# Kernel tuning notes

Hardware: AMD Instinct MI355X
Metric: run time of the kernel (lower is better)

## Reference

```python
import jax, jax.numpy as jnp
import numpy as np

SL, BS, D, H = 2048, 4, 512, 8
NH = D // H  # per-head dim (nhid)
SCALE = np.float32(1.0 / np.sqrt(NH))


def setup_inputs() -> dict:
    key = jax.random.key(0)
    ks = jax.random.split(key, 8)
    s = np.float32(0.02)
    return {
        "input_tensor": jax.random.normal(ks[0], (SL, BS, D), jnp.float32),
        "keys_vector": jax.random.normal(ks[1], (SL, BS, D), jnp.float32),
        "values_vector": jax.random.normal(ks[2], (SL, BS, D), jnp.float32),
        # learned projections: query/keys/values -> num_heads*nhid, plus output proj
        "Wq": jax.random.normal(ks[3], (D, D), jnp.float32) * s,
        "bq": jnp.zeros((D,), jnp.float32),
        "Wk": jax.random.normal(ks[4], (D, D), jnp.float32) * s,
        "bk": jnp.zeros((D,), jnp.float32),
        "Wv": jax.random.normal(ks[5], (D, D), jnp.float32) * s,
        "bv": jnp.zeros((D,), jnp.float32),
        "Wo": jax.random.normal(ks[6], (D, D), jnp.float32) * s,
        "bo": jnp.zeros((D,), jnp.float32),
    }


def reference(input_tensor, keys_vector, values_vector, Wq, bq, Wk, bk, Wv, bv, Wo, bo):
    # Vectorized equivalent of the per-step Python loop with incremental mask
    # (mask=True): query step i attends to keys 0..i -> causal attention.
    q = (input_tensor @ Wq + bq).reshape(SL, BS, H, NH)   # [q,b,h,n]
    k = (keys_vector @ Wk + bk).reshape(SL, BS, H, NH)    # [s,b,h,n]
    v = (values_vector @ Wv + bv).reshape(SL, BS, H, NH)  # [s,b,h,n]
    scores = jnp.einsum('qbhn,sbhn->qsbh', q, k) * SCALE  # [q,s,b,h]
    causal = jnp.tril(jnp.ones((SL, SL), dtype=bool))     # allow s <= q
    scores = jnp.where(causal[:, :, None, None], scores, jnp.float32(-1e9))
    w = jax.nn.softmax(scores, axis=1)                    # softmax over keys s
    out = jnp.einsum('qsbh,sbhn->qbhn', w, v).reshape(SL, BS, D)
    return out @ Wo + bo                                  # [q,b,D]
```

## Files before the change

kernel.cpp:

```cpp
#include <hip/hip_runtime.h>

typedef __attribute__((ext_vector_type(8))) short short8;
typedef __attribute__((ext_vector_type(4))) short short4v;
typedef __attribute__((ext_vector_type(4))) float f32x4;
typedef __attribute__((ext_vector_type(2))) unsigned int uint2v;

constexpr int SL = 2048, BS = 4, D = 512, H = 8, NH = 64;
constexpr int M_ROWS = SL * BS;
constexpr float SCALE = 0.125f;
constexpr float LOG2E = 1.44269504088896340736f;

__device__ __forceinline__ unsigned short f2bf(float f) {
  union { float f; unsigned u; } v; v.f = f;
  unsigned r = v.u + 0x7FFFu + ((v.u >> 16) & 1u);
  return (unsigned short)(r >> 16);
}

__device__ __forceinline__ unsigned cvt_pk_bf16(float a, float b) {
  unsigned r;
  asm("v_cvt_pk_bf16_f32 %0, %1, %2" : "=v"(r) : "v"(a), "v"(b));
  return r;
}

__device__ __forceinline__ float fast_exp2(float x) {
  float r;
  asm("v_exp_f32 %0, %1" : "=v"(r) : "v"(x));
  return r;
}

__device__ __forceinline__ void gl16(const void* g, void* l) {
  __builtin_amdgcn_global_load_lds(
      (const __attribute__((address_space(1))) unsigned int*)g,
      (__attribute__((address_space(3))) unsigned int*)l, 16, 0, 0);
}

__global__ __launch_bounds__(256) void prep_wt(
    const float* __restrict__ w0, const float* __restrict__ w1,
    const float* __restrict__ w2, const float* __restrict__ w3,
    unsigned short* __restrict__ wtb) {
  __shared__ float tl[64][65];
  const int tid = threadIdx.x;
  const int wi = blockIdx.x >> 6, t6 = blockIdx.x & 63;
  const int k0 = (t6 >> 3) * 64, n0 = (t6 & 7) * 64;
  const float* W = wi == 0 ? w0 : (wi == 1 ? w1 : (wi == 2 ? w2 : w3));
  unsigned short* WT = wtb + (size_t)wi * D * D;

#pragma unroll
  for (int i = 0; i < 4; ++i) {
    int k = (tid >> 4) + i * 16, n4 = (tid & 15) * 4;
    f32x4 v = *reinterpret_cast<const f32x4*>(&W[(size_t)(k0 + k) * D + n0 + n4]);
#pragma unroll
    for (int j = 0; j < 4; ++j) tl[n4 + j][k] = v[j];
  }
  __syncthreads();
#pragma unroll
  for (int i = 0; i < 2; ++i) {
    int n = (tid >> 3) + i * 32, k8 = (tid & 7) * 8;
    union { unsigned u[4]; short8 s; } pk;
#pragma unroll
    for (int j = 0; j < 4; ++j)
      pk.u[j] = cvt_pk_bf16(tl[n][k8 + 2 * j], tl[n][k8 + 2 * j + 1]);
    *reinterpret_cast<short8*>(&WT[(size_t)(n0 + n) * D + k0 + k8]) = pk.s;
  }
}

template <bool A_BF16, int OUT_MODE>
__device__ __forceinline__ void gemm_bt_body(const void* __restrict__ Ap,
                                             const unsigned short* __restrict__ BT,
                                             const float* __restrict__ bias,
                                             void* __restrict__ Outp, float scale,
                                             unsigned short* smem) {
  const int tid = threadIdx.x;
  const int brow = blockIdx.x * 128;
  const int bcol = blockIdx.y * 128;
  const int lane = tid & 63;
  const int wid = tid >> 6;
  const int wr = (wid >> 1) * 64;
  const int wc = (wid & 1) * 64;
  const int r = lane & 15;
  const int g = lane >> 4;

  auto a_buf = [&](int b) { return smem + b * 16384; };
  auto b_buf = [&](int b) { return smem + b * 16384 + 8192; };

  f32x4 acc[4][4];
#pragma unroll
  for (int m = 0; m < 4; ++m)
#pragma unroll
    for (int n = 0; n < 4; ++n) acc[m][n] = f32x4{0.f, 0.f, 0.f, 0.f};

  auto STAGE_B = [&](int kt, int bsel) {
    unsigned short* bl = b_buf(bsel);
#pragma unroll
    for (int j = 0; j < 4; ++j) {
      int c = j * 256 + tid;
      int row = c >> 3, c8 = (c & 7) ^ (row & 7);
      gl16(&BT[(size_t)(bcol + row) * D + kt + c8 * 8], &bl[c * 8]);
    }
  };
  auto STAGE_A_LDS = [&](int kt, int bsel) {
    const unsigned short* A = (const unsigned short*)Ap;
    unsigned short* al = a_buf(bsel);
#pragma unroll
    for (int j = 0; j < 4; ++j) {
      int c = j * 256 + tid;
      int row = c >> 3, c8 = (c & 7) ^ (row & 7);
      gl16(&A[(size_t)(brow + row) * D + kt + c8 * 8], &al[c * 8]);
    }
  };
  auto A_LOAD = [&](int kt, f32x4 (&va)[4][2]) {
    const float* A = (const float*)Ap;
#pragma unroll
    for (int j = 0; j < 4; ++j) {
      int c = j * 256 + tid;
      int row = c >> 3, c8 = (c & 7) ^ (row & 7);
      const float* ap = &A[(size_t)(brow + row) * D + kt + c8 * 8];
      va[j][0] = *reinterpret_cast<const f32x4*>(ap);
      va[j][1] = *reinterpret_cast<const f32x4*>(ap + 4);
    }
  };
  auto A_WRITE = [&](f32x4 (&va)[4][2], int bsel) {
    unsigned short* al = a_buf(bsel);
#pragma unroll
    for (int j = 0; j < 4; ++j) {
      int c = j * 256 + tid;
      union { unsigned u[4]; short8 s; } pk;
      pk.u[0] = cvt_pk_bf16(va[j][0][0], va[j][0][1]);
      pk.u[1] = cvt_pk_bf16(va[j][0][2], va[j][0][3]);
      pk.u[2] = cvt_pk_bf16(va[j][1][0], va[j][1][1]);
      pk.u[3] = cvt_pk_bf16(va[j][1][2], va[j][1][3]);
      *reinterpret_cast<short8*>(&al[c * 8]) = pk.s;
    }
  };
  auto COMPUTE = [&](int bsel) {
    const unsigned short* al = a_buf(bsel);
    const unsigned short* bl = b_buf(bsel);
#pragma unroll
    for (int kk2 = 0; kk2 < 2; ++kk2) {
      short8 af[4], bfr[4];
#pragma unroll
      for (int m = 0; m < 4; ++m)
        af[m] = *reinterpret_cast<const short8*>(
            &al[(wr + m * 16 + r) * 64 + (((kk2 * 4 + g) ^ (r & 7)) * 8)]);
#pragma unroll
      for (int n = 0; n < 4; ++n)
        bfr[n] = *reinterpret_cast<const short8*>(
            &bl[(wc + n * 16 + r) * 64 + (((kk2 * 4 + g) ^ (r & 7)) * 8)]);
      __builtin_amdgcn_s_setprio(1);
#pragma unroll
      for (int m = 0; m < 4; ++m)
#pragma unroll
        for (int n = 0; n < 4; ++n)
          acc[m][n] = __builtin_amdgcn_mfma_f32_16x16x32_bf16(af[m], bfr[n], acc[m][n], 0, 0, 0);
      __builtin_amdgcn_s_setprio(0);
    }
  };

  if (A_BF16) {
    STAGE_A_LDS(0, 0);
    STAGE_B(0, 0);
    asm volatile("s_waitcnt vmcnt(0)" ::: "memory");
  } else {
    f32x4 va[4][2];
    A_LOAD(0, va);
    STAGE_B(0, 0);
    asm volatile("s_waitcnt vmcnt(4)" ::: "memory");
    A_WRITE(va, 0);
    asm volatile("s_waitcnt vmcnt(0) lgkmcnt(0)" ::: "memory");
  }
  __builtin_amdgcn_s_barrier();

#pragma unroll
  for (int t = 0; t < 8; ++t) {
    const int cur = t & 1, nxt = cur ^ 1;
    const int ktn = (t + 1) * 64;
    __builtin_amdgcn_sched_barrier(0);
    f32x4 va[4][2];
    if (t < 7) {
      if (A_BF16) {
        STAGE_A_LDS(ktn, nxt);
        STAGE_B(ktn, nxt);
      } else {
        A_LOAD(ktn, va);
        STAGE_B(ktn, nxt);
      }
    }
    __builtin_amdgcn_sched_barrier(0);
    COMPUTE(cur);
    if (t < 7) {
      if (!A_BF16) {
        asm volatile("s_waitcnt vmcnt(4)" ::: "memory");
        A_WRITE(va, nxt);
      }
      asm volatile("s_waitcnt vmcnt(0) lgkmcnt(0)" ::: "memory");
      __builtin_amdgcn_s_barrier();
    }
  }

  if (OUT_MODE == 2) {
    unsigned short* sc = smem;
    const int wr4 = wr >> 2;
#pragma unroll
    for (int m = 0; m < 4; ++m)
#pragma unroll
      for (int n = 0; n < 4; ++n) {
        int col = wc + n * 16 + r;
        float bv = bias[bcol + col];
        int sl = wr4 + m * 4 + g;
#pragma unroll
        for (int rr = 0; rr < 4; ++rr) {
          int c = (rr * 4 + (sl >> 3)) ^ (col & 7);
          sc[col * 128 + c * 8 + (sl & 7)] = f2bf((acc[m][n][rr] + bv) * scale);
        }
      }
    asm volatile("s_waitcnt lgkmcnt(0)" ::: "memory");
    __builtin_amdgcn_s_barrier();
    unsigned short* VT = (unsigned short*)Outp;
#pragma unroll
    for (int i2 = 0; i2 < 2; ++i2) {
      int q = tid * 2 + i2;
      int col = q >> 2, bb = q & 3;
      int gcol = bcol + col, hh = gcol >> 6, nh = gcol & 63;
      size_t gbase = (((size_t)bb * H + hh) * NH + nh) * SL + (brow >> 2);
#pragma unroll
      for (int j = 0; j < 4; ++j) {
        short8 v = *reinterpret_cast<const short8*>(
            &sc[col * 128 + (((bb * 4 + j) ^ (col & 7)) * 8)]);
        *reinterpret_cast<short8*>(&VT[gbase + j * 8]) = v;
      }
    }
  } else {
#pragma unroll
    for (int m = 0; m < 4; ++m)
#pragma unroll
      for (int n = 0; n < 4; ++n) {
        int gcol = bcol + wc + n * 16 + r;
        float bv = bias[gcol];
#pragma unroll
        for (int rr = 0; rr < 4; ++rr) {
          int grow = brow + wr + m * 16 + g * 4 + rr;
          float val = (acc[m][n][rr] + bv) * scale;
          if (OUT_MODE == 0)
            ((float*)Outp)[(size_t)grow * D + gcol] = val;
          else
            ((unsigned short*)Outp)[(size_t)grow * D + gcol] = f2bf(val);
        }
      }
  }
}

__global__ __launch_bounds__(256, 2) void qkv_gemm(
    const float* __restrict__ x0, const float* __restrict__ x1, const float* __restrict__ x2,
    const unsigned short* __restrict__ wtb,
    const float* __restrict__ b0, const float* __restrict__ b1, const float* __restrict__ b2,
    unsigned short* __restrict__ q_out, unsigned short* __restrict__ k_out,
    unsigned short* __restrict__ vt_out) {
  __shared__ __align__(16) unsigned short smem[2 * 16384];
  int z = blockIdx.z;
  const float* X = z == 0 ? x0 : (z == 1 ? x1 : x2);
  const unsigned short* WT = wtb + (size_t)z * D * D;
  const float* B = z == 0 ? b0 : (z == 1 ? b1 : b2);
  float scale = (z == 0) ? SCALE * LOG2E : 1.0f;
  if (z == 2)
    gemm_bt_body<false, 2>(X, WT, B, vt_out, scale, smem);
  else
    gemm_bt_body<false, 1>(X, WT, B, z == 0 ? q_out : k_out, scale, smem);
}

__global__ __launch_bounds__(256, 2) void gemm_oproj(
    const unsigned short* __restrict__ A, const unsigned short* __restrict__ WT,
    const float* __restrict__ B, float* __restrict__ Outp) {
  __shared__ __align__(16) unsigned short smem[2 * 16384];
  gemm_bt_body<true, 0>(A, WT, B, Outp, 1.0f, smem);
}

__global__ __launch_bounds__(256, 2) void flash_attn(
    const unsigned short* __restrict__ Q, const unsigned short* __restrict__ K,
    const unsigned short* __restrict__ Vt, unsigned short* __restrict__ O) {
  __shared__ __align__(16) unsigned short k_lds[2][64 * 64];
  __shared__ __align__(16) unsigned short v_lds[2][64 * 64];
  __shared__ __align__(16) unsigned short p_lds[4][16 * 64];

  const int bid = blockIdx.x;
  const int grp = bid & 7;
  const int i = bid >> 3;
  const int bh = grp * 4 + (i & 3);
  const int b = bh >> 3, h = bh & 7;
  const int t = i >> 2;
  const int qtA = t, qtB = 31 - t;
  const int q0A = qtA * 64, q0B = qtB * 64;

  const int tid = threadIdx.x;
  const int w = tid >> 6, lane = tid & 63;
  const int r = lane & 15, g = lane >> 4;
  const int swz = (r & 7) << 3;

  const unsigned short* Qb = Q + (size_t)b * D + h * NH;
  const unsigned short* Kb = K + (size_t)b * D + h * NH;
  const unsigned short* Vb = Vt + ((size_t)(b * H + h) * NH) * SL;
  unsigned short* Ob = O + (size_t)b * D + h * NH;
  unsigned short* pw = &p_lds[w][0];

  auto STAGE = [&](int kt, int bsel) {
    unsigned short* kl = &k_lds[bsel][0];
    unsigned short* vl = &v_lds[bsel][0];
#pragma unroll
    for (int j = 0; j < 2; ++j) {
      int c = j * 256 + tid;
      int row = c >> 3, c8 = (c & 7) ^ (row & 7);
      gl16(&Kb[(size_t)(kt * 64 + row) * (BS * D) + c8 * 8], &kl[c * 8]);
      gl16(&Vb[(size_t)row * SL + kt * 64 + c8 * 8], &vl[c * 8]);
    }
  };

  STAGE(0, 0);

  short8 qfA[2], qfB[2];
#pragma unroll
  for (int kk = 0; kk < 2; ++kk) {
    qfA[kk] = *reinterpret_cast<const short8*>(
        &Qb[(size_t)(q0A + w * 16 + r) * (BS * D) + kk * 32 + g * 8]);
    qfB[kk] = *reinterpret_cast<const short8*>(
        &Qb[(size_t)(q0B + w * 16 + r) * (BS * D) + kk * 32 + g * 8]);
  }

  f32x4 oa[4];
  float mr, lr;
  auto reset_acc = [&]() {
#pragma unroll
    for (int n = 0; n < 4; ++n) oa[n] = f32x4{0.f, 0.f, 0.f, 0.f};
    mr = -1e30f; lr = 0.f;
  };
  reset_acc();

  auto compute = [&](int q0w, int kt, bool diag, short8(&qf)[2], int bsel) {
    const unsigned short* kl = &k_lds[bsel][0];
    const unsigned short* vl = &v_lds[bsel][0];
    short8 kf[2][4], vt[2][4];
#pragma unroll
    for (int kk = 0; kk < 2; ++kk)
#pragma unroll
      for (int n = 0; n < 4; ++n)
        kf[kk][n] = *reinterpret_cast<const short8*>(
            &kl[(n * 16 + r) * 64 + (((kk * 4 + g) ^ (r & 7)) * 8)]);

    f32x4 s[4];
#pragma unroll
    for (int n = 0; n < 4; ++n) s[n] = f32x4{0.f, 0.f, 0.f, 0.f};
#pragma unroll
    for (int kk = 0; kk < 2; ++kk) {
      __builtin_amdgcn_s_setprio(1);
#pragma unroll
      for (int n = 0; n < 4; ++n)
        s[n] = __builtin_amdgcn_mfma_f32_16x16x32_bf16(kf[kk][n], qf[kk], s[n], 0, 0, 0);
      __builtin_amdgcn_s_setprio(0);
    }

#pragma unroll
    for (int kk = 0; kk < 2; ++kk)
#pragma unroll
      for (int n = 0; n < 4; ++n)
        vt[kk][n] = *reinterpret_cast<const short8*>(
            &vl[(n * 16 + r) * 64 + (((kk * 4 + g) ^ (r & 7)) * 8)]);

    if (diag) {
      int qrow = q0w + r;
#pragma unroll
      for (int n = 0; n < 4; ++n)
#pragma unroll
        for (int rr = 0; rr < 4; ++rr)
          if (kt * 64 + n * 16 + g * 4 + rr > qrow) s[n][rr] = -1e30f;
    }

    float mx = s[0][0];
#pragma unroll
    for (int n = 0; n < 4; ++n)
#pragma unroll
      for (int rr = 0; rr < 4; ++rr)
        if (n | rr) mx = fmaxf(mx, s[n][rr]);
    mx = fmaxf(mx, __shfl_xor(mx, 16));
    mx = fmaxf(mx, __shfl_xor(mx, 32));
    bool need = __any(mx > mr + 8.f);
    float mold = mr;
    float mnew = need ? fmaxf(mold, mx) : mold;
    float ps = 0.f;
#pragma unroll
    for (int n = 0; n < 4; ++n)
#pragma unroll
      for (int rr = 0; rr < 4; ++rr) {
        float p = fast_exp2(s[n][rr] - mnew);
        s[n][rr] = p;
        ps += p;
      }
    ps += __shfl_xor(ps, 16);
    ps += __shfl_xor(ps, 32);
    if (need) {
      float sf = fast_exp2(mold - mnew);
      mr = mnew;
      lr = lr * sf + ps;
#pragma unroll
      for (int n = 0; n < 4; ++n) oa[n] *= sf;
    } else {
      lr += ps;
    }

#pragma unroll
    for (int n = 0; n < 4; ++n) {
      uint2v pk;
      pk.x = cvt_pk_bf16(s[n][0], s[n][1]);
      pk.y = cvt_pk_bf16(s[n][2], s[n][3]);
      *reinterpret_cast<uint2v*>(&pw[r * 64 + ((n * 16 + g * 4) ^ swz)]) = pk;
    }
    asm volatile("s_waitcnt lgkmcnt(0)" ::: "memory");
    __builtin_amdgcn_sched_barrier(0);

    short8 pf[2];
#pragma unroll
    for (int kk = 0; kk < 2; ++kk)
      pf[kk] = *reinterpret_cast<const short8*>(
          &pw[r * 64 + (((kk * 4 + g) ^ (r & 7)) * 8)]);
#pragma unroll
    for (int kk = 0; kk < 2; ++kk) {
      __builtin_amdgcn_s_setprio(1);
#pragma unroll
      for (int n = 0; n < 4; ++n)
        oa[n] = __builtin_amdgcn_mfma_f32_16x16x32_bf16(vt[kk][n], pf[kk], oa[n], 0, 0, 0);
      __builtin_amdgcn_s_setprio(0);
    }
  };

  auto finalize = [&](int q0) {
    float inv = 1.0f / lr;
#pragma unroll
    for (int n = 0; n < 4; ++n) {
      uint2v pk;
      pk.x = cvt_pk_bf16(oa[n][0] * inv, oa[n][1] * inv);
      pk.y = cvt_pk_bf16(oa[n][2] * inv, oa[n][3] * inv);
      *reinterpret_cast<uint2v*>(&pw[r * 64 + ((n * 16 + g * 4) ^ swz)]) = pk;
    }
    asm volatile("s_waitcnt lgkmcnt(0)" ::: "memory");
    __builtin_amdgcn_sched_barrier(0);
#pragma unroll
    for (int i2 = 0; i2 < 2; ++i2) {
      int c = i2 * 64 + lane;
      int row = c >> 3, c8 = c & 7;
      short8 v = *reinterpret_cast<const short8*>(&pw[row * 64 + c8 * 8]);
      *reinterpret_cast<short8*>(
          &Ob[(size_t)(q0 + w * 16 + row) * (BS * D) + ((c8 ^ (row & 7)) * 8)]) = v;
    }
  };

  int ph = 0;
  for (int kt = 0; kt <= qtA; ++kt, ++ph) {
    asm volatile("s_waitcnt vmcnt(0)" ::: "memory");
    __builtin_amdgcn_s_barrier();
    __builtin_amdgcn_sched_barrier(0);
    int np = ph + 1;
    if (np < 33) STAGE(np <= qtA ? np : np - qtA - 1, np & 1);
    compute(q0A + w * 16, kt, kt == qtA, qfA, ph & 1);
  }
  finalize(q0A);
  reset_acc();
  for (int kt = 0; kt <= qtB; ++kt, ++ph) {
    asm volatile("s_waitcnt vmcnt(0)" ::: "memory");
    __builtin_amdgcn_s_barrier();
    __builtin_amdgcn_sched_barrier(0);
    int np = ph + 1;
    if (np < 33) STAGE(np - qtA - 1, np & 1);
    compute(q0B + w * 16, kt, kt == qtB, qfB, ph & 1);
  }
  finalize(q0B);
}

extern "C" void kernel_launch(void* const* d_in, const int* in_sizes, int n_in,
                              void* d_out, int out_size, void* d_ws, size_t ws_size,
                              hipStream_t stream) {
  const float* x  = (const float*)d_in[0];
  const float* kx = (const float*)d_in[1];
  const float* vx = (const float*)d_in[2];
  const float* Wq = (const float*)d_in[3];
  const float* bq = (const float*)d_in[4];
  const float* Wk = (const float*)d_in[5];
  const float* bk = (const float*)d_in[6];
  const float* Wv = (const float*)d_in[7];
  const float* bv = (const float*)d_in[8];
  const float* Wo = (const float*)d_in[9];
  const float* bo = (const float*)d_in[10];

  unsigned short* ws = (unsigned short*)d_ws;
  unsigned short* qb  = ws;
  unsigned short* kb  = ws + (size_t)M_ROWS * D;
  unsigned short* vtb = ws + (size_t)M_ROWS * D * 2;
  unsigned short* wtb = ws + (size_t)M_ROWS * D * 3;

  prep_wt<<<dim3(256), dim3(256), 0, stream>>>(Wq, Wk, Wv, Wo, wtb);
  qkv_gemm<<<dim3(64, 4, 3), dim3(256), 0, stream>>>(x, kx, vx, wtb, bq, bk, bv,
                                                     qb, kb, vtb);
  flash_attn<<<dim3(512), dim3(256), 0, stream>>>(qb, kb, vtb, qb);
  gemm_oproj<<<dim3(64, 4, 1), dim3(256), 0, stream>>>(qb, wtb + (size_t)3 * D * D,
                                                       bo, (float*)d_out);
}
```

Baseline: 86.80 us.

## Split paired-tile attention blocks into one q-tile per block with longest-first order

Flash attention previously gave each block two complementary query tiles (t and 31-t) so every block did equal causal work. Now each of 1024 blocks handles a single 64-row query tile, and block indices are mapped so the longest tiles are dispatched first. Launch bounds are raised to 4 blocks per SIMD-group for more occupancy. The max and sum reductions are rewritten as trees to shorten dependency chains. This trades static load balance for more parallelism and dynamic scheduling, and it adds more per-block setup and Q loads.

```diff
diff --git a/kernel.cpp b/kernel.cpp
--- a/kernel.cpp
+++ b/kernel.cpp
@@ -274,7 +274,7 @@
   gemm_bt_body<true, 0>(A, WT, B, Outp, 1.0f, smem);
 }
 
-__global__ __launch_bounds__(256, 2) void flash_attn(
+__global__ __launch_bounds__(256, 4) void flash_attn(
     const unsigned short* __restrict__ Q, const unsigned short* __restrict__ K,
     const unsigned short* __restrict__ Vt, unsigned short* __restrict__ O) {
   __shared__ __align__(16) unsigned short k_lds[2][64 * 64];
@@ -282,13 +282,12 @@
   __shared__ __align__(16) unsigned short p_lds[4][16 * 64];
 
   const int bid = blockIdx.x;
-  const int grp = bid & 7;
-  const int i = bid >> 3;
-  const int bh = grp * 4 + (i & 3);
+  const int s = bid >> 5, idx = bid & 31;
+  const int grp = idx & 7;
+  const int bh = grp * 4 + (idx >> 3);
   const int b = bh >> 3, h = bh & 7;
-  const int t = i >> 2;
-  const int qtA = t, qtB = 31 - t;
-  const int q0A = qtA * 64, q0B = qtB * 64;
+  const int qt = (s < 8) ? 31 - s : (s < 16) ? s + 8 : (s < 24) ? 31 - s : s - 24;
+  const int q0 = qt * 64;
 
   const int tid = threadIdx.x;
   const int w = tid >> 6, lane = tid & 63;
@@ -315,25 +314,24 @@
 
   STAGE(0, 0);
 
-  short8 qfA[2], qfB[2];
-#pragma unroll
-  for (int kk = 0; kk < 2; ++kk) {
-    qfA[kk] = *reinterpret_cast<const short8*>(
-        &Qb[(size_t)(q0A + w * 16 + r) * (BS * D) + kk * 32 + g * 8]);
-    qfB[kk] = *reinterpret_cast<const short8*>(
-        &Qb[(size_t)(q0B + w * 16 + r) * (BS * D) + kk * 32 + g * 8]);
-  }
+  short8 qf[2];
+#pragma unroll
+  for (int kk = 0; kk < 2; ++kk)
+    qf[kk] = *reinterpret_cast<const short8*>(
+        &Qb[(size_t)(q0 + w * 16 + r) * (BS * D) + kk * 32 + g * 8]);
 
   f32x4 oa[4];
-  float mr, lr;
-  auto reset_acc = [&]() {
-#pragma unroll
-    for (int n = 0; n < 4; ++n) oa[n] = f32x4{0.f, 0.f, 0.f, 0.f};
-    mr = -1e30f; lr = 0.f;
-  };
-  reset_acc();
-
-  auto compute = [&](int q0w, int kt, bool diag, short8(&qf)[2], int bsel) {
+#pragma unroll
+  for (int n = 0; n < 4; ++n) oa[n] = f32x4{0.f, 0.f, 0.f, 0.f};
+  float mr = -1e30f, lr = 0.f;
+
+  for (int kt = 0; kt <= qt; ++kt) {
+    asm volatile("s_waitcnt vmcnt(0)" ::: "memory");
+    __builtin_amdgcn_s_barrier();
+    __builtin_amdgcn_sched_barrier(0);
+    if (kt + 1 <= qt) STAGE(kt + 1, (kt + 1) & 1);
+
+    const int bsel = kt & 1;
     const unsigned short* kl = &k_lds[bsel][0];
     const unsigned short* vl = &v_lds[bsel][0];
     short8 kf[2][4], vt[2][4];
@@ -344,15 +342,15 @@
         kf[kk][n] = *reinterpret_cast<const short8*>(
             &kl[(n * 16 + r) * 64 + (((kk * 4 + g) ^ (r & 7)) * 8)]);
 
-    f32x4 s[4];
-#pragma unroll
-    for (int n = 0; n < 4; ++n) s[n] = f32x4{0.f, 0.f, 0.f, 0.f};
+    f32x4 sv[4];
+#pragma unroll
+    for (int n = 0; n < 4; ++n) sv[n] = f32x4{0.f, 0.f, 0.f, 0.f};
 #pragma unroll
     for (int kk = 0; kk < 2; ++kk) {
       __builtin_amdgcn_s_setprio(1);
 #pragma unroll
       for (int n = 0; n < 4; ++n)
-        s[n] = __builtin_amdgcn_mfma_f32_16x16x32_bf16(kf[kk][n], qf[kk], s[n], 0, 0, 0);
+        sv[n] = __builtin_amdgcn_mfma_f32_16x16x32_bf16(kf[kk][n], qf[kk], sv[n], 0, 0, 0);
       __builtin_amdgcn_s_setprio(0);
     }
 
@@ -363,35 +361,36 @@
         vt[kk][n] = *reinterpret_cast<const short8*>(
             &vl[(n * 16 + r) * 64 + (((kk * 4 + g) ^ (r & 7)) * 8)]);
 
-    if (diag) {
-      int qrow = q0w + r;
+    if (kt == qt) {
+      int qrow = q0 + w * 16 + r;
 #pragma unroll
       for (int n = 0; n < 4; ++n)
 #pragma unroll
         for (int rr = 0; rr < 4; ++rr)
-          if (kt * 64 + n * 16 + g * 4 + rr > qrow) s[n][rr] = -1e30f;
-    }
-
-    float mx = s[0][0];
-#pragma unroll
-    for (int n = 0; n < 4; ++n)
-#pragma unroll
-      for (int rr = 0; rr < 4; ++rr)
-        if (n | rr) mx = fmaxf(mx, s[n][rr]);
+          if (kt * 64 + n * 16 + g * 4 + rr > qrow) sv[n][rr] = -1e30f;
+    }
+
+    float t0 = fmaxf(fmaxf(sv[0][0], sv[0][1]), sv[0][2]);
+    float t1 = fmaxf(fmaxf(sv[0][3], sv[1][0]), sv[1][1]);
+    float t2 = fmaxf(fmaxf(sv[1][2], sv[1][3]), sv[2][0]);
+    float t3 = fmaxf(fmaxf(sv[2][1], sv[2][2]), sv[2][3]);
+    float t4 = fmaxf(fmaxf(sv[3][0], sv[3][1]), sv[3][2]);
+    float mx = fmaxf(fmaxf(fmaxf(t0, t1), fmaxf(t2, t3)), fmaxf(t4, sv[3][3]));
     mx = fmaxf(mx, __shfl_xor(mx, 16));
     mx = fmaxf(mx, __shfl_xor(mx, 32));
     bool need = __any(mx > mr + 8.f);
     float mold = mr;
     float mnew = need ? fmaxf(mold, mx) : mold;
-    float ps = 0.f;
 #pragma unroll
     for (int n = 0; n < 4; ++n)
 #pragma unroll
-      for (int rr = 0; rr < 4; ++rr) {
-        float p = fast_exp2(s[n][rr] - mnew);
-        s[n][rr] = p;
-        ps += p;
-      }
+      for (int rr = 0; rr < 4; ++rr)
+        sv[n][rr] = fast_exp2(sv[n][rr] - mnew);
+    float a0 = (sv[0][0] + sv[0][1]) + (sv[0][2] + sv[0][3]);
+    float a1 = (sv[1][0] + sv[1][1]) + (sv[1][2] + sv[1][3]);
+    float a2 = (sv[2][0] + sv[2][1]) + (sv[2][2] + sv[2][3]);
+    float a3 = (sv[3][0] + sv[3][1]) + (sv[3][2] + sv[3][3]);
+    float ps = (a0 + a1) + (a2 + a3);
     ps += __shfl_xor(ps, 16);
     ps += __shfl_xor(ps, 32);
     if (need) {
@@ -407,8 +406,8 @@
 #pragma unroll
     for (int n = 0; n < 4; ++n) {
       uint2v pk;
-      pk.x = cvt_pk_bf16(s[n][0], s[n][1]);
-      pk.y = cvt_pk_bf16(s[n][2], s[n][3]);
+      pk.x = cvt_pk_bf16(sv[n][0], sv[n][1]);
+      pk.y = cvt_pk_bf16(sv[n][2], sv[n][3]);
       *reinterpret_cast<uint2v*>(&pw[r * 64 + ((n * 16 + g * 4) ^ swz)]) = pk;
     }
     asm volatile("s_waitcnt lgkmcnt(0)" ::: "memory");
@@ -427,9 +426,9 @@
         oa[n] = __builtin_amdgcn_mfma_f32_16x16x32_bf16(vt[kk][n], pf[kk], oa[n], 0, 0, 0);
       __builtin_amdgcn_s_setprio(0);
     }
-  };
-
-  auto finalize = [&](int q0) {
+  }
+
+  {
     float inv = 1.0f / lr;
 #pragma unroll
     for (int n = 0; n < 4; ++n) {
@@ -448,28 +447,7 @@
       *reinterpret_cast<short8*>(
           &Ob[(size_t)(q0 + w * 16 + row) * (BS * D) + ((c8 ^ (row & 7)) * 8)]) = v;
     }
-  };
-
-  int ph = 0;
-  for (int kt = 0; kt <= qtA; ++kt, ++ph) {
-    asm volatile("s_waitcnt vmcnt(0)" ::: "memory");
-    __builtin_amdgcn_s_barrier();
-    __builtin_amdgcn_sched_barrier(0);
-    int np = ph + 1;
-    if (np < 33) STAGE(np <= qtA ? np : np - qtA - 1, np & 1);
-    compute(q0A + w * 16, kt, kt == qtA, qfA, ph & 1);
-  }
-  finalize(q0A);
-  reset_acc();
-  for (int kt = 0; kt <= qtB; ++kt, ++ph) {
-    asm volatile("s_waitcnt vmcnt(0)" ::: "memory");
-    __builtin_amdgcn_s_barrier();
-    __builtin_amdgcn_sched_barrier(0);
-    int np = ph + 1;
-    if (np < 33) STAGE(np - qtA - 1, np & 1);
-    compute(q0B + w * 16, kt, kt == qtB, qfB, ph & 1);
-  }
-  finalize(q0B);
+  }
 }
 
 extern "C" void kernel_launch(void* const* d_in, const int* in_sizes, int n_in,
@@ -496,7 +474,7 @@
   prep_wt<<<dim3(256), dim3(256), 0, stream>>>(Wq, Wk, Wv, Wo, wtb);
   qkv_gemm<<<dim3(64, 4, 3), dim3(256), 0, stream>>>(x, kx, vx, wtb, bq, bk, bv,
                                                      qb, kb, vtb);
-  flash_attn<<<dim3(512), dim3(256), 0, stream>>>(qb, kb, vtb, qb);
+  flash_attn<<<dim3(1024), dim3(256), 0, stream>>>(qb, kb, vtb, qb);
   gemm_oproj<<<dim3(64, 4, 1), dim3(256), 0, stream>>>(qb, wtb + (size_t)3 * D * D,
                                                        bo, (float*)d_out);
 }
```

Result: no change. 85.19 us (-1.9%).
